# Optimization experiments

Hardware: AMD Instinct MI355X
Metric: run time of the kernel (lower is better)

Reference implementation:

```python
import jax, jax.numpy as jnp
import numpy as np

DIM = 192  # init dim; input channels = 2*DIM, output channels = DIM
EPS = 1e-5


def setup_inputs() -> dict:
    key = jax.random.key(0)
    k1, k2 = jax.random.split(key)
    x = jax.random.normal(k1, (2, 16, 32, 32, 2 * DIM), dtype=jnp.float32)
    W = jax.random.normal(k2, (2 * DIM, 8 * DIM), dtype=jnp.float32) * 0.02
    gamma = jnp.ones((2 * DIM,), dtype=jnp.float32)
    beta = jnp.zeros((2 * DIM,), dtype=jnp.float32)
    return {"x": x, "W": W, "gamma": gamma, "beta": beta}


def reference(x, W, gamma, beta):
    dim = DIM
    b, d, h, w, c = x.shape  # c == 2*dim
    # LayerNorm over last dim (biased variance, as torch)
    mu = jnp.mean(x, axis=-1, keepdims=True)
    var = jnp.var(x, axis=-1, keepdims=True)
    xn = (x - mu) * jax.lax.rsqrt(var + EPS) * gamma + beta
    # Linear expansion 2*dim -> 8*dim (no bias)
    xe = jnp.einsum('bdhwc,ce->bdhwe', xn, W)  # (b,d,h,w,8*dim)
    ch = lambda i: xe[..., i * dim:(i + 1) * dim]
    z = jnp.zeros((b, d, h, w, dim), dtype=xe.dtype)
    # Faithful to the torch code: parities (0,1,0) and (0,0,1) are written
    # are NEVER written (stay zero). Index = pd*4 + ph*2 + pw.
    grid = jnp.stack([
        ch(0), ch(6),  # (0,0,0), (0,0,1)
        ch(5), z,      # (0,1,0), (0,1,1)
        ch(1), ch(4),  # (1,0,0), (1,0,1)
        z,     ch(7),  # (1,1,0), (1,1,1)
    ], axis=4)  # (b,d,h,w,8,dim)
    grid = grid.reshape(b, d, h, w, 2, 2, 2, dim)
    # interleave parity axes: (b, d,pd, h,ph, w,pw, dim) -> (b,2d,2h,2w,dim)
    out = grid.transpose(0, 1, 4, 2, 5, 3, 6, 7).reshape(b, 2 * d, 2 * h, 2 * w, dim)
    return out
```

## Files before the change

### kernel.cpp

```cpp
#include <hip/hip_runtime.h>
#include <hip/hip_bf16.h>
#include <stdint.h>


typedef __attribute__((ext_vector_type(4))) float f32x4;
typedef __attribute__((ext_vector_type(8))) short s16x8;
typedef __attribute__((ext_vector_type(4))) unsigned short u16x4;
typedef const __attribute__((address_space(1))) void gvoid_t;
typedef __attribute__((address_space(3))) void lvoid_t;

__device__ __forceinline__ int ob_of_p(int p) {
    const int w = p & 31, h = (p >> 5) & 31, d = (p >> 10) & 15, b = p >> 14;
    return b * 25165824 + d * 1572864 + h * 24576 + w * 384;
}

__device__ __forceinline__ unsigned short f2bf(float f) {
    unsigned u = __builtin_bit_cast(unsigned, f);
    u += 0x7fffu + ((u >> 16) & 1u);
    return (unsigned short)(u >> 16);
}


__global__ __launch_bounds__(256) void lnwt_kernel(const float* __restrict__ x,
                                                   const float* __restrict__ gamma,
                                                   const float* __restrict__ beta,
                                                   const float* __restrict__ W,
                                                   float* __restrict__ outf,
                                                   unsigned short* __restrict__ xn,
                                                   unsigned short* __restrict__ wt) {
    if (blockIdx.x >= 8192) {
        const int t = (blockIdx.x - 8192) * 256 + threadIdx.x;
        const int k = t % 384;
        const int n = t / 384;
        const int s = n / 192;
        const int oc = (s < 2 ? s : s + 2) * 192 + (n % 192);
        wt[(size_t)n * 384 + k] = f2bf(W[(size_t)k * 1536 + oc]);
        return;
    }
    const int wv = threadIdx.x >> 6;
    const int l  = threadIdx.x & 63;
    const int p  = blockIdx.x * 4 + wv;
    const float* row = x + (size_t)p * 384;
    f32x4 v0 = *(const f32x4*)(row + l * 4);
    f32x4 v1 = {0.f, 0.f, 0.f, 0.f};
    if (l < 32) v1 = *(const f32x4*)(row + 256 + l * 4);
    float s  = v0[0]+v0[1]+v0[2]+v0[3] + v1[0]+v1[1]+v1[2]+v1[3];
    float s2 = v0[0]*v0[0]+v0[1]*v0[1]+v0[2]*v0[2]+v0[3]*v0[3]
             + v1[0]*v1[0]+v1[1]*v1[1]+v1[2]*v1[2]+v1[3]*v1[3];
    #pragma unroll
    for (int off = 32; off >= 1; off >>= 1) {
        s  += __shfl_xor(s,  off);
        s2 += __shfl_xor(s2, off);
    }
    const float mu = s * (1.f / 384.f);
    const float rs = rsqrtf(s2 * (1.f / 384.f) - mu * mu + 1e-5f);
    unsigned short* dst = xn + (size_t)p * 384;
    f32x4 g0 = *(const f32x4*)(gamma + l * 4);
    f32x4 b0 = *(const f32x4*)(beta  + l * 4);
    u16x4 o0;
    #pragma unroll
    for (int j = 0; j < 4; ++j) o0[j] = f2bf((v0[j] - mu) * rs * g0[j] + b0[j]);
    *(u16x4*)(dst + l * 4) = o0;
    if (l < 32) {
        f32x4 g1 = *(const f32x4*)(gamma + 256 + l * 4);
        f32x4 b1 = *(const f32x4*)(beta  + 256 + l * 4);
        u16x4 o1;
        #pragma unroll
        for (int j = 0; j < 4; ++j) o1[j] = f2bf((v1[j] - mu) * rs * g1[j] + b1[j]);
        *(u16x4*)(dst + 256 + l * 4) = o1;
    }
    if (l < 48) {
        const int ob = ob_of_p(p);
        const f32x4 z = {0.f, 0.f, 0.f, 0.f};
        __builtin_nontemporal_store(z, (f32x4*)(outf + ob + 12480  + l * 4));
        __builtin_nontemporal_store(z, (f32x4*)(outf + ob + 798720 + l * 4));
    }
}

__global__ __launch_bounds__(256) void gemm7_kernel(const unsigned short* __restrict__ xn,
                                                    const unsigned short* __restrict__ wt,
                                                    float* __restrict__ outf) {
    __shared__ char lds[65536];
    const char* xb = (const char*)xn;
    const char* wb = (const char*)wt;
    const int tid = threadIdx.x;
    const int wv = tid >> 6, l = tid & 63;
    int bid = blockIdx.x;
    bid = (bid & 7) * 288 + (bid >> 3);
    const int mt = bid / 9, nt = bid % 9;
    const int m0 = mt * 128, n0 = nt * 128;
    const int wm = wv >> 1, wn = wv & 1;

    size_t srcA[4], srcB[4];
    int ldsA[4], ldsB[4];
    #pragma unroll
    for (int i = 0; i < 4; ++i) {
        const int r = wv * 32 + i * 8 + (l >> 3);
        const int swz = ((l & 7) * 16) ^ ((r & 7) << 4);
        srcA[i] = (size_t)(m0 + r) * 768 + swz;
        srcB[i] = (size_t)(n0 + r) * 768 + swz;
        ldsA[i] = (wv * 32 + i * 8) * 128;
        ldsB[i] = 16384 + (wv * 32 + i * 8) * 128;
    }

    f32x4 acc[4][4];
    const f32x4 fz = {0.f, 0.f, 0.f, 0.f};
    #pragma unroll
    for (int m = 0; m < 4; ++m)
        #pragma unroll
        for (int n = 0; n < 4; ++n) acc[m][n] = fz;

    int arow[4], brow[4];
    #pragma unroll
    for (int i = 0; i < 4; ++i) {
        arow[i] = wm * 64 + i * 16 + (l & 15);
        brow[i] = wn * 64 + i * 16 + (l & 15);
    }
    const int kbyte0 = (l >> 4) * 16;

    #pragma unroll
    for (int i = 0; i < 4; ++i) {
        __builtin_amdgcn_global_load_lds((gvoid_t*)(xb + srcA[i]),
                                         (lvoid_t*)(lds + ldsA[i]), 16, 0, 0);
        __builtin_amdgcn_global_load_lds((gvoid_t*)(wb + srcB[i]),
                                         (lvoid_t*)(lds + ldsB[i]), 16, 0, 0);
    }

    #pragma unroll
    for (int t = 0; t < 6; ++t) {
        const int cur = (t & 1) * 32768;
        const int nxt = 32768 - cur;
        if (t < 5) {
            #pragma unroll
            for (int i = 0; i < 4; ++i) {
                __builtin_amdgcn_global_load_lds((gvoid_t*)(xb + srcA[i] + (t + 1) * 128),
                                                 (lvoid_t*)(lds + nxt + ldsA[i]), 16, 0, 0);
                __builtin_amdgcn_global_load_lds((gvoid_t*)(wb + srcB[i] + (t + 1) * 128),
                                                 (lvoid_t*)(lds + nxt + ldsB[i]), 16, 0, 0);
            }
            asm volatile("s_waitcnt vmcnt(8)\n\ts_barrier" ::: "memory");
        } else {
            asm volatile("s_waitcnt vmcnt(0)\n\ts_barrier" ::: "memory");
        }
        #pragma unroll
        for (int kk = 0; kk < 2; ++kk) {
            const int kbyte = kbyte0 + kk * 64;
            s16x8 a[4], b[4];
            #pragma unroll
            for (int m = 0; m < 4; ++m)
                a[m] = *(const s16x8*)(lds + cur + arow[m] * 128 + (kbyte ^ ((arow[m] & 7) << 4)));
            #pragma unroll
            for (int n = 0; n < 4; ++n)
                b[n] = *(const s16x8*)(lds + cur + 16384 + brow[n] * 128 + (kbyte ^ ((brow[n] & 7) << 4)));
            #pragma unroll
            for (int m = 0; m < 4; ++m)
                #pragma unroll
                for (int n = 0; n < 4; ++n)
                    acc[m][n] = __builtin_amdgcn_mfma_f32_16x16x32_bf16(a[m], b[n], acc[m][n], 0, 0, 0);
        }
        asm volatile("s_waitcnt lgkmcnt(0)\n\ts_barrier" ::: "memory");
    }

    int coladd[4];
    #pragma unroll
    for (int n = 0; n < 4; ++n) {
        const int gnb = n0 + wn * 64 + n * 16;
        const int s = gnb / 192;
        int d;
        if      (s == 0) d = 0;
        else if (s == 1) d = 786432;
        else if (s == 2) d = 786624;
        else if (s == 3) d = 12288;
        else if (s == 4) d = 192;
        else             d = 798912;
        coladd[n] = d + (gnb % 192) + (l & 15);
    }
    const int pb = m0 + wm * 64 + (l >> 4) * 4;
    #pragma unroll
    for (int m = 0; m < 4; ++m) {
        #pragma unroll
        for (int r = 0; r < 4; ++r) {
            const int ob = ob_of_p(pb + m * 16 + r);
            #pragma unroll
            for (int n = 0; n < 4; ++n)
                __builtin_nontemporal_store(acc[m][n][r], outf + ob + coladd[n]);
        }
    }
}


__global__ __launch_bounds__(256) void ln_kernel(const float* __restrict__ x,
                                                 const float* __restrict__ gamma,
                                                 const float* __restrict__ beta,
                                                 float* __restrict__ outf) {
    const int wv = threadIdx.x >> 6;
    const int l  = threadIdx.x & 63;
    const int p  = blockIdx.x * 4 + wv;
    const float* row = x + (size_t)p * 384;
    f32x4 v0 = *(const f32x4*)(row + l * 4);
    f32x4 v1 = {0.f, 0.f, 0.f, 0.f};
    if (l < 32) v1 = *(const f32x4*)(row + 256 + l * 4);
    float s  = v0[0]+v0[1]+v0[2]+v0[3] + v1[0]+v1[1]+v1[2]+v1[3];
    float s2 = v0[0]*v0[0]+v0[1]*v0[1]+v0[2]*v0[2]+v0[3]*v0[3]
             + v1[0]*v1[0]+v1[1]*v1[1]+v1[2]*v1[2]+v1[3]*v1[3];
    #pragma unroll
    for (int off = 32; off >= 1; off >>= 1) {
        s  += __shfl_xor(s,  off);
        s2 += __shfl_xor(s2, off);
    }
    const float mu = s * (1.f / 384.f);
    const float rs = rsqrtf(s2 * (1.f / 384.f) - mu * mu + 1e-5f);
    unsigned short* dst = (unsigned short*)(outf + ob_of_p(p) + 12480);
    f32x4 g0 = *(const f32x4*)(gamma + l * 4);
    f32x4 b0 = *(const f32x4*)(beta  + l * 4);
    u16x4 o0;
    #pragma unroll
    for (int j = 0; j < 4; ++j) o0[j] = f2bf((v0[j] - mu) * rs * g0[j] + b0[j]);
    *(u16x4*)(dst + l * 4) = o0;
    if (l < 32) {
        f32x4 g1 = *(const f32x4*)(gamma + 256 + l * 4);
        f32x4 b1 = *(const f32x4*)(beta  + 256 + l * 4);
        u16x4 o1;
        #pragma unroll
        for (int j = 0; j < 4; ++j) o1[j] = f2bf((v1[j] - mu) * rs * g1[j] + b1[j]);
        *(u16x4*)(dst + 256 + l * 4) = o1;
    }
}

__global__ __launch_bounds__(256) void wt_kernel(const float* __restrict__ W,
                                                 float* __restrict__ outf) {
    const int t = blockIdx.x * 256 + threadIdx.x;
    const int k = t % 384;
    const int n = t / 384;
    const int s = n / 192;
    const int oc = (s < 2 ? s : s + 2) * 192 + (n % 192);
    const float v = W[(size_t)k * 1536 + oc];
    unsigned short* dst = (unsigned short*)(outf + ob_of_p(n) + 798720);
    dst[k] = f2bf(v);
}

__global__ __launch_bounds__(256) void gemm_kernel(float* __restrict__ outf) {
    __shared__ char lds[32768];
    const char* gbase = (const char*)outf;
    const int tid = threadIdx.x;
    const int wv = tid >> 6, l = tid & 63;
    int bid = blockIdx.x;
    bid = (bid & 7) * 288 + (bid >> 3);
    const int mt = bid / 9, nt = bid % 9;
    const int m0 = mt * 128, n0 = nt * 128;
    size_t srcA[4], srcB[4];
    int ldsA[4], ldsB[4];
    #pragma unroll
    for (int i = 0; i < 4; ++i) {
        const int r = wv * 32 + i * 8 + (l >> 3);
        const int swz = ((l & 7) * 16) ^ ((r & 7) << 4);
        srcA[i] = (size_t)(ob_of_p(m0 + r) + 12480)  * 4 + swz;
        srcB[i] = (size_t)(ob_of_p(n0 + r) + 798720) * 4 + swz;
        ldsA[i] = (wv * 32 + i * 8) * 128;
        ldsB[i] = 16384 + (wv * 32 + i * 8) * 128;
    }
    f32x4 acc[4][4];
    const f32x4 fz = {0.f, 0.f, 0.f, 0.f};
    #pragma unroll
    for (int m = 0; m < 4; ++m)
        #pragma unroll
        for (int n = 0; n < 4; ++n) acc[m][n] = fz;
    const int wm = wv >> 1, wn = wv & 1;
    int arow[4], brow[4];
    #pragma unroll
    for (int i = 0; i < 4; ++i) {
        arow[i] = wm * 64 + i * 16 + (l & 15);
        brow[i] = wn * 64 + i * 16 + (l & 15);
    }
    const int kbyte0 = (l >> 4) * 16;
    for (int t = 0; t < 6; ++t) {
        const int kb = t * 128;
        #pragma unroll
        for (int i = 0; i < 4; ++i)
            __builtin_amdgcn_global_load_lds((gvoid_t*)(gbase + srcA[i] + kb),
                                             (lvoid_t*)(lds + ldsA[i]), 16, 0, 0);
        #pragma unroll
        for (int i = 0; i < 4; ++i)
            __builtin_amdgcn_global_load_lds((gvoid_t*)(gbase + srcB[i] + kb),
                                             (lvoid_t*)(lds + ldsB[i]), 16, 0, 0);
        __syncthreads();
        #pragma unroll
        for (int kk = 0; kk < 2; ++kk) {
            const int kbyte = kbyte0 + kk * 64;
            s16x8 a[4], b[4];
            #pragma unroll
            for (int m = 0; m < 4; ++m)
                a[m] = *(const s16x8*)(lds + arow[m] * 128 + (kbyte ^ ((arow[m] & 7) << 4)));
            #pragma unroll
            for (int n = 0; n < 4; ++n)
                b[n] = *(const s16x8*)(lds + 16384 + brow[n] * 128 + (kbyte ^ ((brow[n] & 7) << 4)));
            #pragma unroll
            for (int m = 0; m < 4; ++m)
                #pragma unroll
                for (int n = 0; n < 4; ++n)
                    acc[m][n] = __builtin_amdgcn_mfma_f32_16x16x32_bf16(a[m], b[n], acc[m][n], 0, 0, 0);
        }
        __syncthreads();
    }
    int coladd[4];
    #pragma unroll
    for (int n = 0; n < 4; ++n) {
        const int gnb = n0 + wn * 64 + n * 16;
        const int s = gnb / 192;
        int d;
        if      (s == 0) d = 0;
        else if (s == 1) d = 786432;
        else if (s == 2) d = 786624;
        else if (s == 3) d = 12288;
        else if (s == 4) d = 192;
        else             d = 798912;
        coladd[n] = d + (gnb % 192) + (l & 15);
    }
    const int pb = m0 + wm * 64 + (l >> 4) * 4;
    #pragma unroll
    for (int m = 0; m < 4; ++m) {
        #pragma unroll
        for (int r = 0; r < 4; ++r) {
            const int ob = ob_of_p(pb + m * 16 + r);
            #pragma unroll
            for (int n = 0; n < 4; ++n)
                outf[ob + coladd[n]] = acc[m][n][r];
        }
    }
}

__global__ __launch_bounds__(256) void zero_kernel(float* __restrict__ outf) {
    const int idx = blockIdx.x * 256 + threadIdx.x;
    const int f4 = idx % 48;
    const int pr = (idx / 48) & 1;
    const int p  = idx / 96;
    const f32x4 z = {0.f, 0.f, 0.f, 0.f};
    *(f32x4*)(outf + ob_of_p(p) + (pr ? 798720 : 12480) + f4 * 4) = z;
}


extern "C" void kernel_launch(void* const* d_in, const int* in_sizes, int n_in,
                              void* d_out, int out_size, void* d_ws, size_t ws_size,
                              hipStream_t stream) {
    const float* x     = (const float*)d_in[0];
    const float* W     = (const float*)d_in[1];
    const float* gamma = (const float*)d_in[2];
    const float* beta  = (const float*)d_in[3];
    float* out = (float*)d_out;
    const size_t need = 25165824 + 884736;
    if (ws_size >= need) {
        unsigned short* xn = (unsigned short*)d_ws;
        unsigned short* wt = (unsigned short*)((char*)d_ws + 25165824);
        lnwt_kernel <<<9920, 256, 0, stream>>>(x, gamma, beta, W, out, xn, wt);
        gemm7_kernel<<<2304, 256, 0, stream>>>(xn, wt, out);
    } else {
        ln_kernel  <<<8192,  256, 0, stream>>>(x, gamma, beta, out);
        wt_kernel  <<<1728,  256, 0, stream>>>(W, out);
        gemm_kernel<<<2304,  256, 0, stream>>>(out);
        zero_kernel<<<12288, 256, 0, stream>>>(out);
    }
}
```

Before: 69.32 us.

## Fuse LayerNorm into GEMM with LDS-resident normalized A tile across all N tiles

```diff
diff --git a/kernel.cpp b/kernel.cpp
--- a/kernel.cpp
+++ b/kernel.cpp
@@ -5,6 +5,7 @@
 
 typedef __attribute__((ext_vector_type(4))) float f32x4;
 typedef __attribute__((ext_vector_type(8))) short s16x8;
+typedef __attribute__((ext_vector_type(4))) unsigned int u32x4;
 typedef __attribute__((ext_vector_type(4))) unsigned short u16x4;
 typedef const __attribute__((address_space(1))) void gvoid_t;
 typedef __attribute__((address_space(3))) void lvoid_t;
@@ -21,87 +22,85 @@
 }
 
 
-__global__ __launch_bounds__(256) void lnwt_kernel(const float* __restrict__ x,
-                                                   const float* __restrict__ gamma,
-                                                   const float* __restrict__ beta,
-                                                   const float* __restrict__ W,
-                                                   float* __restrict__ outf,
-                                                   unsigned short* __restrict__ xn,
-                                                   unsigned short* __restrict__ wt) {
-    if (blockIdx.x >= 8192) {
-        const int t = (blockIdx.x - 8192) * 256 + threadIdx.x;
-        const int k = t % 384;
-        const int n = t / 384;
-        const int s = n / 192;
-        const int oc = (s < 2 ? s : s + 2) * 192 + (n % 192);
-        wt[(size_t)n * 384 + k] = f2bf(W[(size_t)k * 1536 + oc]);
-        return;
-    }
-    const int wv = threadIdx.x >> 6;
-    const int l  = threadIdx.x & 63;
-    const int p  = blockIdx.x * 4 + wv;
-    const float* row = x + (size_t)p * 384;
-    f32x4 v0 = *(const f32x4*)(row + l * 4);
-    f32x4 v1 = {0.f, 0.f, 0.f, 0.f};
-    if (l < 32) v1 = *(const f32x4*)(row + 256 + l * 4);
-    float s  = v0[0]+v0[1]+v0[2]+v0[3] + v1[0]+v1[1]+v1[2]+v1[3];
-    float s2 = v0[0]*v0[0]+v0[1]*v0[1]+v0[2]*v0[2]+v0[3]*v0[3]
-             + v1[0]*v1[0]+v1[1]*v1[1]+v1[2]*v1[2]+v1[3]*v1[3];
-    #pragma unroll
-    for (int off = 32; off >= 1; off >>= 1) {
-        s  += __shfl_xor(s,  off);
-        s2 += __shfl_xor(s2, off);
-    }
-    const float mu = s * (1.f / 384.f);
-    const float rs = rsqrtf(s2 * (1.f / 384.f) - mu * mu + 1e-5f);
-    unsigned short* dst = xn + (size_t)p * 384;
-    f32x4 g0 = *(const f32x4*)(gamma + l * 4);
-    f32x4 b0 = *(const f32x4*)(beta  + l * 4);
-    u16x4 o0;
-    #pragma unroll
-    for (int j = 0; j < 4; ++j) o0[j] = f2bf((v0[j] - mu) * rs * g0[j] + b0[j]);
-    *(u16x4*)(dst + l * 4) = o0;
-    if (l < 32) {
-        f32x4 g1 = *(const f32x4*)(gamma + 256 + l * 4);
-        f32x4 b1 = *(const f32x4*)(beta  + 256 + l * 4);
-        u16x4 o1;
-        #pragma unroll
-        for (int j = 0; j < 4; ++j) o1[j] = f2bf((v1[j] - mu) * rs * g1[j] + b1[j]);
-        *(u16x4*)(dst + 256 + l * 4) = o1;
-    }
-    if (l < 48) {
-        const int ob = ob_of_p(p);
-        const f32x4 z = {0.f, 0.f, 0.f, 0.f};
-        __builtin_nontemporal_store(z, (f32x4*)(outf + ob + 12480  + l * 4));
-        __builtin_nontemporal_store(z, (f32x4*)(outf + ob + 798720 + l * 4));
-    }
-}
-
-__global__ __launch_bounds__(256) void gemm7_kernel(const unsigned short* __restrict__ xn,
+__global__ __launch_bounds__(256) void wt2_kernel(const float* __restrict__ W,
+                                                  unsigned short* __restrict__ wt) {
+    const int t = blockIdx.x * 256 + threadIdx.x;
+    const int k = t % 384;
+    const int n = t / 384;
+    const int s = n / 192;
+    const int oc = (s < 2 ? s : s + 2) * 192 + (n % 192);
+    wt[(size_t)n * 384 + k] = f2bf(W[(size_t)k * 1536 + oc]);
+}
+
+__global__ __launch_bounds__(256) void fused_kernel(const float* __restrict__ x,
+                                                    const float* __restrict__ gamma,
+                                                    const float* __restrict__ beta,
                                                     const unsigned short* __restrict__ wt,
                                                     float* __restrict__ outf) {
-    __shared__ char lds[65536];
-    const char* xb = (const char*)xn;
+    extern __shared__ char lds[];
     const char* wb = (const char*)wt;
     const int tid = threadIdx.x;
     const int wv = tid >> 6, l = tid & 63;
-    int bid = blockIdx.x;
-    bid = (bid & 7) * 288 + (bid >> 3);
-    const int mt = bid / 9, nt = bid % 9;
-    const int m0 = mt * 128, n0 = nt * 128;
+    const int m0 = blockIdx.x * 128;
     const int wm = wv >> 1, wn = wv & 1;
 
-    size_t srcA[4], srcB[4];
-    int ldsA[4], ldsB[4];
+    size_t srcB[4]; int ldsB[4];
     #pragma unroll
     for (int i = 0; i < 4; ++i) {
-        const int r = wv * 32 + i * 8 + (l >> 3);
-        const int swz = ((l & 7) * 16) ^ ((r & 7) << 4);
-        srcA[i] = (size_t)(m0 + r) * 768 + swz;
-        srcB[i] = (size_t)(n0 + r) * 768 + swz;
-        ldsA[i] = (wv * 32 + i * 8) * 128;
-        ldsB[i] = 16384 + (wv * 32 + i * 8) * 128;
-    }
+        const int rB = wv * 32 + i * 8 + (l >> 3);
+        srcB[i] = (size_t)rB * 768 + (((l & 7) * 16) ^ ((rB & 7) << 4));
+        ldsB[i] = 98304 + (wv * 32 + i * 8) * 128;
+    }
+
+    const int r = tid >> 1, h = tid & 1;
+    const float* xrow = x + (size_t)(m0 + r) * 384 + h * 192;
+    float s = 0.f, s2 = 0.f;
+    #pragma unroll
+    for (int bq = 0; bq < 6; ++bq) {
+        f32x4 v[8];
+        #pragma unroll
+        for (int q = 0; q < 8; ++q) v[q] = *(const f32x4*)(xrow + bq * 32 + q * 4);
+        #pragma unroll
+        for (int q = 0; q < 8; ++q) {
+            s  += v[q][0] + v[q][1] + v[q][2] + v[q][3];
+            s2 += v[q][0]*v[q][0] + v[q][1]*v[q][1] + v[q][2]*v[q][2] + v[q][3]*v[q][3];
+        }
+    }
+    s  += __shfl_xor(s,  1);
+    s2 += __shfl_xor(s2, 1);
+    const float mu = s * (1.f / 384.f);
+    const float rs = rsqrtf(s2 * (1.f / 384.f) - mu * mu + 1e-5f);
+    const int swzr = (r & 7) << 4;
+    #pragma unroll
+    for (int bq = 0; bq < 6; ++bq) {
+        f32x4 v[8], g[8], b[8];
+        #pragma unroll
+        for (int q = 0; q < 8; ++q) {
+            v[q] = *(const f32x4*)(xrow + bq * 32 + q * 4);
+            g[q] = *(const f32x4*)(gamma + h * 192 + bq * 32 + q * 4);
+            b[q] = *(const f32x4*)(beta  + h * 192 + bq * 32 + q * 4);
+        }
+        #pragma unroll
+        for (int j = 0; j < 4; ++j) {
+            u32x4 c;
+            #pragma unroll
+            for (int k = 0; k < 4; ++k) {
+                const int q = j * 2 + (k >> 1);
+                const int e = (k & 1) * 2;
+                const float f0 = fmaf((v[q][e]     - mu) * rs, g[q][e],     b[q][e]);
+                const float f1 = fmaf((v[q][e + 1] - mu) * rs, g[q][e + 1], b[q][e + 1]);
+                c[k] = (unsigned)f2bf(f0) | ((unsigned)f2bf(f1) << 16);
+            }
+            const int ch = h * 24 + bq * 4 + j;
+            *(u32x4*)(lds + r * 768 + ((ch * 16) ^ swzr)) = c;
+        }
+    }
+
+    #pragma unroll
+    for (int i = 0; i < 4; ++i)
+        __builtin_amdgcn_global_load_lds((gvoid_t*)(wb + srcB[i]),
+                                         (lvoid_t*)(lds + ldsB[i]), 16, 0, 0);
+    __syncthreads();
 
     f32x4 acc[4][4];
     const f32x4 fz = {0.f, 0.f, 0.f, 0.f};
@@ -117,73 +116,80 @@
         brow[i] = wn * 64 + i * 16 + (l & 15);
     }
     const int kbyte0 = (l >> 4) * 16;
-
-    #pragma unroll
-    for (int i = 0; i < 4; ++i) {
-        __builtin_amdgcn_global_load_lds((gvoid_t*)(xb + srcA[i]),
-                                         (lvoid_t*)(lds + ldsA[i]), 16, 0, 0);
-        __builtin_amdgcn_global_load_lds((gvoid_t*)(wb + srcB[i]),
-                                         (lvoid_t*)(lds + ldsB[i]), 16, 0, 0);
-    }
-
-    #pragma unroll
-    for (int t = 0; t < 6; ++t) {
-        const int cur = (t & 1) * 32768;
-        const int nxt = 32768 - cur;
-        if (t < 5) {
-            #pragma unroll
-            for (int i = 0; i < 4; ++i) {
-                __builtin_amdgcn_global_load_lds((gvoid_t*)(xb + srcA[i] + (t + 1) * 128),
-                                                 (lvoid_t*)(lds + nxt + ldsA[i]), 16, 0, 0);
-                __builtin_amdgcn_global_load_lds((gvoid_t*)(wb + srcB[i] + (t + 1) * 128),
-                                                 (lvoid_t*)(lds + nxt + ldsB[i]), 16, 0, 0);
+    const int pb = m0 + wm * 64 + (l >> 4) * 4;
+    const int obz = ob_of_p(m0 + (tid >> 1)) + ((tid & 1) ? 798720 : 12480);
+
+    for (int nt = 0; nt < 9; ++nt) {
+        const int n0 = nt * 128;
+        #pragma unroll
+        for (int t = 0; t < 6; ++t) {
+            const int cb = t & 1;
+            const int sstep = nt * 6 + t;
+            if (sstep < 53) {
+                const int nnt = (t < 5) ? nt : nt + 1;
+                const int ntt = (t < 5) ? t + 1 : 0;
+                #pragma unroll
+                for (int i = 0; i < 4; ++i)
+                    __builtin_amdgcn_global_load_lds(
+                        (gvoid_t*)(wb + (size_t)nnt * 98304 + srcB[i] + ntt * 128),
+                        (lvoid_t*)(lds + (cb ^ 1) * 16384 + ldsB[i]), 16, 0, 0);
+                asm volatile("s_waitcnt vmcnt(4)\n\ts_barrier" ::: "memory");
+            } else {
+                asm volatile("s_waitcnt vmcnt(0)\n\ts_barrier" ::: "memory");
             }
-            asm volatile("s_waitcnt vmcnt(8)\n\ts_barrier" ::: "memory");
-        } else {
-            asm volatile("s_waitcnt vmcnt(0)\n\ts_barrier" ::: "memory");
-        }
-        #pragma unroll
-        for (int kk = 0; kk < 2; ++kk) {
-            const int kbyte = kbyte0 + kk * 64;
-            s16x8 a[4], b[4];
-            #pragma unroll
-            for (int m = 0; m < 4; ++m)
-                a[m] = *(const s16x8*)(lds + cur + arow[m] * 128 + (kbyte ^ ((arow[m] & 7) << 4)));
-            #pragma unroll
-            for (int n = 0; n < 4; ++n)
-                b[n] = *(const s16x8*)(lds + cur + 16384 + brow[n] * 128 + (kbyte ^ ((brow[n] & 7) << 4)));
-            #pragma unroll
-            for (int m = 0; m < 4; ++m)
+            #pragma unroll
+            for (int kk = 0; kk < 2; ++kk) {
+                const int kb2 = kbyte0 + kk * 64;
+                s16x8 a[4], b[4];
+                #pragma unroll
+                for (int m = 0; m < 4; ++m)
+                    a[m] = *(const s16x8*)(lds + arow[m] * 768 +
+                                           ((t * 128 + kb2) ^ ((arow[m] & 7) << 4)));
                 #pragma unroll
                 for (int n = 0; n < 4; ++n)
-                    acc[m][n] = __builtin_amdgcn_mfma_f32_16x16x32_bf16(a[m], b[n], acc[m][n], 0, 0, 0);
-        }
-        asm volatile("s_waitcnt lgkmcnt(0)\n\ts_barrier" ::: "memory");
-    }
-
-    int coladd[4];
-    #pragma unroll
-    for (int n = 0; n < 4; ++n) {
-        const int gnb = n0 + wn * 64 + n * 16;
-        const int s = gnb / 192;
-        int d;
-        if      (s == 0) d = 0;
-        else if (s == 1) d = 786432;
-        else if (s == 2) d = 786624;
-        else if (s == 3) d = 12288;
-        else if (s == 4) d = 192;
-        else             d = 798912;
-        coladd[n] = d + (gnb % 192) + (l & 15);
-    }
-    const int pb = m0 + wm * 64 + (l >> 4) * 4;
-    #pragma unroll
-    for (int m = 0; m < 4; ++m) {
-        #pragma unroll
-        for (int r = 0; r < 4; ++r) {
-            const int ob = ob_of_p(pb + m * 16 + r);
-            #pragma unroll
-            for (int n = 0; n < 4; ++n)
-                __builtin_nontemporal_store(acc[m][n][r], outf + ob + coladd[n]);
+                    b[n] = *(const s16x8*)(lds + 98304 + cb * 16384 + brow[n] * 128 +
+                                           (kb2 ^ ((brow[n] & 7) << 4)));
+                #pragma unroll
+                for (int m = 0; m < 4; ++m)
+                    #pragma unroll
+                    for (int n = 0; n < 4; ++n)
+                        acc[m][n] = __builtin_amdgcn_mfma_f32_16x16x32_bf16(a[m], b[n], acc[m][n], 0, 0, 0);
+            }
+            asm volatile("s_waitcnt lgkmcnt(0)\n\ts_barrier" ::: "memory");
+        }
+
+        int coladd[4];
+        #pragma unroll
+        for (int n = 0; n < 4; ++n) {
+            const int gnb = n0 + wn * 64 + n * 16;
+            const int sl = gnb / 192;
+            const int d = (sl == 0) ? 0
+                        : (sl == 1) ? 786432
+                        : (sl == 2) ? 786624
+                        : (sl == 3) ? 12288
+                        : (sl == 4) ? 192
+                        :             798912;
+            coladd[n] = d + (gnb % 192) + (l & 15);
+        }
+        #pragma unroll
+        for (int m = 0; m < 4; ++m) {
+            #pragma unroll
+            for (int rr = 0; rr < 4; ++rr) {
+                const int ob = ob_of_p(pb + m * 16 + rr);
+                #pragma unroll
+                for (int n = 0; n < 4; ++n)
+                    __builtin_nontemporal_store(acc[m][n][rr], outf + ob + coladd[n]);
+            }
+        }
+        #pragma unroll
+        for (int m = 0; m < 4; ++m)
+            #pragma unroll
+            for (int n = 0; n < 4; ++n) acc[m][n] = fz;
+        if (nt < 8) {
+            const f32x4 z = {0.f, 0.f, 0.f, 0.f};
+            #pragma unroll
+            for (int j = 0; j < 6; ++j)
+                __builtin_nontemporal_store(z, (f32x4*)(outf + obz + (nt * 6 + j) * 4));
         }
     }
 }
@@ -347,12 +353,11 @@
     const float* gamma = (const float*)d_in[2];
     const float* beta  = (const float*)d_in[3];
     float* out = (float*)d_out;
-    const size_t need = 25165824 + 884736;
+    const size_t need = 884736;
     if (ws_size >= need) {
-        unsigned short* xn = (unsigned short*)d_ws;
-        unsigned short* wt = (unsigned short*)((char*)d_ws + 25165824);
-        lnwt_kernel <<<9920, 256, 0, stream>>>(x, gamma, beta, W, out, xn, wt);
-        gemm7_kernel<<<2304, 256, 0, stream>>>(xn, wt, out);
+        unsigned short* wt = (unsigned short*)d_ws;
+        wt2_kernel  <<<1728, 256, 0, stream>>>(W, wt);
+        fused_kernel<<<256,  256, 131072, stream>>>(x, gamma, beta, wt, out);
     } else {
         ln_kernel  <<<8192,  256, 0, stream>>>(x, gamma, beta, out);
         wt_kernel  <<<1728,  256, 0, stream>>>(W, out);
```

New measurement: 206.8 us. 198% more time.
